# Performance work log

Hardware: AMD Instinct MI355X
Metric: run time of the kernel (lower is better)

The kernel has to match this reference:

```python
import jax, jax.numpy as jnp
import numpy as np

# Dimensions (match init_kwargs / input_specs)
B, C, H, W = 16, 96, 224, 224
COUT = 96
PH, PW = 16, 16          # patch_size (== patch_stride, non-overlapping)
KH, KW = 3, 3            # patch_kernel and output_kernel
PAD = 1                  # padding
GH, GW = H // PH, W // PW
P = GH * GW              # num_patches = 196


def setup_inputs() -> dict:
    key = jax.random.key(0)
    k1, k2, k3 = jax.random.split(key, 3)
    x = jax.random.normal(k1, (B, C, H, W), dtype=jnp.float32)
    # kaiming-normal-ish init scales (fan_in over trailing dims, as torch does)
    pf = jax.random.normal(k2, (C, P, 1, KH, KW), dtype=jnp.float32) * np.float32(np.sqrt(2.0 / (P * KH * KW)))
    of = jax.random.normal(k3, (COUT, C, KH, KW), dtype=jnp.float32) * np.float32(np.sqrt(2.0 / (C * KH * KW)))
    return {"x": x, "patch_filters": pf, "output_filters": of}


def _self_conv2d(x, patch_filters):
    """Locally-connected per-patch depthwise conv.

    x: (B, C, H, W); patch_filters: (C, P, 1, KH, KW).
    Each of the P non-overlapping PHxPW patches of each channel is convolved
    with its own KHxKW kernel (padding=PAD, stride=1), then patches are
    reassembled into the full (B, C, H, W) map.
    """
    # (B, C, GH, PH, GW, PW) -> (B, C, GH, GW, PH, PW) -> (B, C*P, PH, PW)
    xp = x.reshape(B, C, GH, PH, GW, PW).transpose(0, 1, 2, 4, 3, 5).reshape(B, C * P, PH, PW)
    k = patch_filters.reshape(C * P, 1, KH, KW)
    y = jax.lax.conv_general_dilated(
        xp, k,
        window_strides=(1, 1),
        padding=[(PAD, PAD), (PAD, PAD)],
        feature_group_count=C * P,
        dimension_numbers=("NCHW", "OIHW", "NCHW"),
    )  # (B, C*P, PH, PW) since 3x3 conv with pad 1 preserves size
    return y.reshape(B, C, GH, GW, PH, PW).transpose(0, 1, 2, 4, 3, 5).reshape(B, C, H, W)


def reference(x, patch_filters, output_filters):
    # input already at (max_input_height, max_input_width) -> F.pad is a no-op
    sa = _self_conv2d(x, patch_filters)
    out = jax.lax.conv_general_dilated(
        sa, output_filters,
        window_strides=(1, 1),
        padding=[(PAD, PAD), (PAD, PAD)],
        dimension_numbers=("NCHW", "OIHW", "NCHW"),
    )  # (B, COUT, H, W)
    return jax.nn.gelu(out, approximate=False)  # torch nn.GELU() = exact erf gelu
```

## Files before the change

kernel.cpp:

```cpp
#include <hip/hip_runtime.h>
#include <hip/hip_bf16.h>

#define B_    16
#define C_    96
#define H_    224
#define W_    224
#define COUT_ 96
#define GH_   14
#define GW_   14
#define P_    196
#define HW_   (H_*W_)
#define NCH_  12

#define AS1 __attribute__((address_space(1)))
#define AS3 __attribute__((address_space(3)))

typedef __attribute__((ext_vector_type(8))) unsigned short ushort8;
typedef __attribute__((ext_vector_type(8))) short        short8;
typedef __attribute__((ext_vector_type(4))) float        f32x4;

__device__ __forceinline__ unsigned short f2bf(float f) {
    union { __hip_bfloat16 h; unsigned short u; } cv;
    cv.h = __float2bfloat16(f);
    return cv.u;
}

__global__ __launch_bounds__(256) void prep_ofb(const float* __restrict__ of,
                                                unsigned short* __restrict__ ofb,
                                                unsigned short* __restrict__ zp) {
    if (blockIdx.x == 0 && threadIdx.x < 128) zp[threadIdx.x] = 0;
    int idx = blockIdx.x * 256 + threadIdx.x;
    if (idx < 9 * 96 * 96) {
        int tap = idx / (96 * 96);
        int r   = idx % (96 * 96);
        int cout = r / 96, c = r % 96;
        ofb[idx] = f2bf(of[((size_t)cout * 96 + c) * 9 + tap]);
    }
}

__global__ __launch_bounds__(256) void sa_kernel(const float* __restrict__ x,
                                                 const float* __restrict__ pf,
                                                 unsigned short* __restrict__ sa) {
    int bid   = blockIdx.x;
    int patch = bid % P_;
    int b     = bid / P_;
    int gh = patch / GW_, gw = patch % GW_;
    int t  = threadIdx.x;
    int py = t >> 4, px = t & 15;
    int y  = gh * 16 + py, xx = gw * 16 + px;

    __shared__ float xs[2][8][256];

    const float* xp0 = x + (size_t)b * C_ * HW_ + (size_t)y * W_ + xx;

    float lf[8];
    #pragma unroll
    for (int ch = 0; ch < 8; ++ch) lf[ch] = xp0[(size_t)ch * HW_];

    for (int cc = 0; cc < NCH_; ++cc) {
        int buf = cc & 1;
        #pragma unroll
        for (int ch = 0; ch < 8; ++ch) xs[buf][ch][t] = lf[ch];
        __syncthreads();
        if (cc < NCH_ - 1) {
            #pragma unroll
            for (int ch = 0; ch < 8; ++ch)
                lf[ch] = xp0[(size_t)((cc + 1) * 8 + ch) * HW_];
        }

        ushort8 v;
        #pragma unroll
        for (int ch = 0; ch < 8; ++ch) {
            const float* wgt = pf + ((size_t)(cc * 8 + ch) * P_ + patch) * 9;
            float a = 0.f;
            #pragma unroll
            for (int dy = -1; dy <= 1; ++dy) {
                int yy = py + dy;
                if ((unsigned)yy < 16u) {
                    #pragma unroll
                    for (int dx = -1; dx <= 1; ++dx) {
                        int xq = px + dx;
                        if ((unsigned)xq < 16u)
                            a = fmaf(xs[buf][ch][yy * 16 + xq],
                                     wgt[(dy + 1) * 3 + (dx + 1)], a);
                    }
                }
            }
            v[ch] = f2bf(a);
        }
        *(ushort8*)&sa[(((size_t)(b * NCH_ + cc) * H_ + y) * W_ + xx) * 8] = v;
    }
}

__global__ __launch_bounds__(256, 2) void conv2_mfma(const unsigned short* __restrict__ sa,
                                                     const unsigned short* __restrict__ ofb,
                                                     const unsigned short* __restrict__ zp,
                                                     float* __restrict__ out) {
    int bid0 = blockIdx.x;
    int bid  = (bid0 % 8) * (3136 / 8) + bid0 / 8;
    int patch = bid % P_;
    int b     = bid / P_;
    int gh = patch / GW_, gw = patch % GW_;
    int y0 = gh * 16, x0 = gw * 16;

    int t = threadIdx.x;
    int w = t >> 6, l = t & 63;
    int mrow = l & 15, kgrp = l >> 4;

    __shared__ ushort8 at8[4096];

    #pragma unroll
    for (int i = 0; i < 16; ++i) {
        int v = t + i * 256;
        const unsigned short* src = zp;
        if (v < 3888) {
            int hpx = v / 12, ccl = v - hpx * 12;
            int gy = y0 - 1 + hpx / 18, gx = x0 - 1 + hpx % 18;
            if ((unsigned)gy < (unsigned)H_ && (unsigned)gx < (unsigned)W_)
                src = &sa[(((size_t)(b * NCH_ + ccl) * H_ + gy) * W_ + gx) * 8];
        }
        __builtin_amdgcn_global_load_lds((const AS1 unsigned int*)src,
                                         (AS3 unsigned int*)&at8[v], 16, 0, 0);
    }

    f32x4 acc[4][6];
    #pragma unroll
    for (int mi = 0; mi < 4; ++mi)
        #pragma unroll
        for (int ni = 0; ni < 6; ++ni)
            acc[mi][ni] = (f32x4)0.f;

    __syncthreads();

    const unsigned short* at = (const unsigned short*)at8;

    #pragma unroll 1
    for (int tap = 0; tap < 9; ++tap) {
        int ky = tap / 3, kx = tap % 3;
        const unsigned short* bofs0 = ofb + tap * (96 * 96) + kgrp * 8;
        #pragma unroll
        for (int cs = 0; cs < 3; ++cs) {
            short8 bf[6];
            #pragma unroll
            for (int ni = 0; ni < 6; ++ni)
                bf[ni] = *(const short8*)&bofs0[(ni * 16 + mrow) * 96 + cs * 32];
            #pragma unroll
            for (int mi = 0; mi < 4; ++mi) {
                short8 af = *(const short8*)&at[((w * 4 + mi + ky) * 18 + kx + mrow) * 96
                                                + cs * 32 + kgrp * 8];
                #pragma unroll
                for (int ni = 0; ni < 6; ++ni)
                    acc[mi][ni] = __builtin_amdgcn_mfma_f32_16x16x32_bf16(
                        af, bf[ni], acc[mi][ni], 0, 0, 0);
            }
        }
    }

    #pragma unroll
    for (int mi = 0; mi < 4; ++mi) {
        int gy = y0 + w * 4 + mi;
        #pragma unroll
        for (int ni = 0; ni < 6; ++ni) {
            int cout = ni * 16 + mrow;
            f32x4 gv;
            #pragma unroll
            for (int j = 0; j < 4; ++j) {
                float vv = acc[mi][ni][j];
                gv[j] = 0.5f * vv * (1.0f + erff(vv * 0.70710678118f));
            }
            *(f32x4*)&out[((size_t)b * COUT_ + cout) * HW_ + (size_t)gy * W_ +
                          x0 + kgrp * 4] = gv;
        }
    }
}

extern "C" void kernel_launch(void* const* d_in, const int* in_sizes, int n_in,
                              void* d_out, int out_size, void* d_ws, size_t ws_size,
                              hipStream_t stream) {
    const float* x  = (const float*)d_in[0];
    const float* pf = (const float*)d_in[1];
    const float* of = (const float*)d_in[2];
    float* out = (float*)d_out;

    unsigned short* sa  = (unsigned short*)d_ws;
    unsigned short* ofb = (unsigned short*)((char*)d_ws + 154140672);
    unsigned short* zp  = (unsigned short*)((char*)d_ws + 154306560);

    prep_ofb<<<324, 256, 0, stream>>>(of, ofb, zp);
    sa_kernel<<<B_ * P_, 256, 0, stream>>>(x, pf, sa);
    conv2_mfma<<<B_ * P_, 256, 0, stream>>>(sa, ofb, zp, out);
}
```

Measured before the change: 412.5 us.

## Pad LDS pixel stride and pre-swizzle weights into MFMA fragment order

The LDS activation tile now stores each halo pixel with a 13-chunk (104-element) stride instead of 12, padding rows so the per-lane fragment reads spread across banks rather than conflicting. The bf16 output filters are reordered in the prep kernel into exact per-lane MFMA B-fragment order, so each lane's weight load is a contiguous, fully coalesced 16-byte read. This costs slightly more LDS (one extra load iteration with zero-filled padding slots) and a more complex index computation in the prep kernel.

```diff
diff --git a/kernel.cpp b/kernel.cpp
--- a/kernel.cpp
+++ b/kernel.cpp
@@ -26,15 +26,19 @@
 }
 
 __global__ __launch_bounds__(256) void prep_ofb(const float* __restrict__ of,
-                                                unsigned short* __restrict__ ofb,
+                                                unsigned short* __restrict__ ofb3,
                                                 unsigned short* __restrict__ zp) {
     if (blockIdx.x == 0 && threadIdx.x < 128) zp[threadIdx.x] = 0;
-    int idx = blockIdx.x * 256 + threadIdx.x;
-    if (idx < 9 * 96 * 96) {
-        int tap = idx / (96 * 96);
-        int r   = idx % (96 * 96);
-        int cout = r / 96, c = r % 96;
-        ofb[idx] = f2bf(of[((size_t)cout * 96 + c) * 9 + tap]);
+    int e = blockIdx.x * 256 + threadIdx.x;
+    if (e < 82944) {
+        int j    = e & 7;
+        int l    = (e >> 3) & 63;
+        int ni   = (e >> 9) % 6;
+        int cs   = (e / 3072) % 3;
+        int tap  = e / 9216;
+        int cout = ni * 16 + (l & 15);
+        int c    = cs * 32 + (l >> 4) * 8 + j;
+        ofb3[e] = f2bf(of[((size_t)cout * 96 + c) * 9 + tap]);
     }
 }
 
@@ -93,7 +97,7 @@
 }
 
 __global__ __launch_bounds__(256, 2) void conv2_mfma(const unsigned short* __restrict__ sa,
-                                                     const unsigned short* __restrict__ ofb,
+                                                     const unsigned short* __restrict__ ofb3,
                                                      const unsigned short* __restrict__ zp,
                                                      float* __restrict__ out) {
     int bid0 = blockIdx.x;
@@ -107,17 +111,19 @@
     int w = t >> 6, l = t & 63;
     int mrow = l & 15, kgrp = l >> 4;
 
-    __shared__ ushort8 at8[4096];
+    __shared__ ushort8 at8[4352];
 
     #pragma unroll
-    for (int i = 0; i < 16; ++i) {
+    for (int i = 0; i < 17; ++i) {
         int v = t + i * 256;
         const unsigned short* src = zp;
-        if (v < 3888) {
-            int hpx = v / 12, ccl = v - hpx * 12;
-            int gy = y0 - 1 + hpx / 18, gx = x0 - 1 + hpx % 18;
-            if ((unsigned)gy < (unsigned)H_ && (unsigned)gx < (unsigned)W_)
-                src = &sa[(((size_t)(b * NCH_ + ccl) * H_ + gy) * W_ + gx) * 8];
+        if (v < 4212) {
+            int hpx = v / 13, ccl = v - hpx * 13;
+            if (ccl < 12) {
+                int gy = y0 - 1 + hpx / 18, gx = x0 - 1 + hpx % 18;
+                if ((unsigned)gy < (unsigned)H_ && (unsigned)gx < (unsigned)W_)
+                    src = &sa[(((size_t)(b * NCH_ + ccl) * H_ + gy) * W_ + gx) * 8];
+            }
         }
         __builtin_amdgcn_global_load_lds((const AS1 unsigned int*)src,
                                          (AS3 unsigned int*)&at8[v], 16, 0, 0);
@@ -137,17 +143,17 @@
     #pragma unroll 1
     for (int tap = 0; tap < 9; ++tap) {
         int ky = tap / 3, kx = tap % 3;
-        const unsigned short* bofs0 = ofb + tap * (96 * 96) + kgrp * 8;
+        const unsigned short* bofs0 = ofb3 + (size_t)tap * 9216 + l * 8;
         #pragma unroll
         for (int cs = 0; cs < 3; ++cs) {
             short8 bf[6];
             #pragma unroll
             for (int ni = 0; ni < 6; ++ni)
-                bf[ni] = *(const short8*)&bofs0[(ni * 16 + mrow) * 96 + cs * 32];
+                bf[ni] = *(const short8*)&bofs0[(cs * 6 + ni) * 512];
             #pragma unroll
             for (int mi = 0; mi < 4; ++mi) {
-                short8 af = *(const short8*)&at[((w * 4 + mi + ky) * 18 + kx + mrow) * 96
-                                                + cs * 32 + kgrp * 8];
+                short8 af = *(const short8*)&at[((w * 4 + mi + ky) * 18 + kx + mrow) * 104
+                                                + (cs * 4 + kgrp) * 8];
                 #pragma unroll
                 for (int ni = 0; ni < 6; ++ni)
                     acc[mi][ni] = __builtin_amdgcn_mfma_f32_16x16x32_bf16(
@@ -182,11 +188,11 @@
     const float* of = (const float*)d_in[2];
     float* out = (float*)d_out;
 
-    unsigned short* sa  = (unsigned short*)d_ws;
-    unsigned short* ofb = (unsigned short*)((char*)d_ws + 154140672);
-    unsigned short* zp  = (unsigned short*)((char*)d_ws + 154306560);
+    unsigned short* sa   = (unsigned short*)d_ws;
+    unsigned short* ofb3 = (unsigned short*)((char*)d_ws + 154140672);
+    unsigned short* zp   = (unsigned short*)((char*)d_ws + 154306560);
 
-    prep_ofb<<<324, 256, 0, stream>>>(of, ofb, zp);
+    prep_ofb<<<324, 256, 0, stream>>>(of, ofb3, zp);
     sa_kernel<<<B_ * P_, 256, 0, stream>>>(x, pf, sa);
-    conv2_mfma<<<B_ * P_, 256, 0, stream>>>(sa, ofb, zp, out);
+    conv2_mfma<<<B_ * P_, 256, 0, stream>>>(sa, ofb3, zp, out);
 }
```

Measured after the change: 386.5 us. 1.07x faster.
